# Kernel optimization log

Hardware: AMD Instinct MI355X
Metric: run time of the kernel (lower is better)

## Reference

```python
import jax, jax.numpy as jnp
import numpy as np

LEAKY_SLOPE = 0.2
ALPHA, BETA = 1.0, 0.1
CLAMP_MAX = 40.0

N_NODES, N_FEAT = 20000, 128
N_EDGES, N_QUERY = 320000, 200000
B = 512            # boundary matrix size
DIM = 8            # 'dimension' hyperparam


def setup_inputs() -> dict:
    key = jax.random.key(0)
    ks = jax.random.split(key, 20)
    sc = 1.0 / np.sqrt(B)
    inp = {
        'x': jax.random.normal(ks[0], (N_NODES, N_FEAT), jnp.float32),
        'L0': jax.random.normal(ks[1], (B, B), jnp.float32) * sc,
        'L1': jax.random.normal(ks[2], (B, B), jnp.float32) * sc,
        'edge_index': jax.random.randint(ks[3], (2, N_EDGES), 0, N_NODES),
        'total_edges': jax.random.randint(ks[4], (N_QUERY, 2), 0, N_NODES),
        # learned params (Linear weights stored as [in, out])
        'conv1_W': jax.random.normal(ks[5], (N_FEAT, 64), jnp.float32) * 0.05,
        'conv1_b': jnp.zeros((64,), jnp.float32),
        'conv2_W': jax.random.normal(ks[6], (64, 32), jnp.float32) * 0.05,
        'conv2_b': jnp.zeros((32,), jnp.float32),
        'weights_sim': jax.random.normal(ks[7], (2 * B, DIM), jnp.float32) * 0.05,
        'embeddings_sim': jax.random.normal(ks[8], (N_FEAT, 2 * B), jnp.float32) * 0.05,
        'weights_off_diagonal': jax.random.normal(ks[9], (B, B), jnp.float32) * sc,
        'weights_L_0': jax.random.normal(ks[10], (B, 32), jnp.float32) * 0.05,
        'weights_L_1': jax.random.normal(ks[11], (B, 32), jnp.float32) * 0.05,
        'lin1_W': jax.random.normal(ks[12], (DIM + 32, 32), jnp.float32) * 0.1,
        'lin1_b': jnp.zeros((32,), jnp.float32),
        'lin_W': jax.random.normal(ks[13], (32, 1), jnp.float32) * 0.1,
        'lin_b': jnp.zeros((1,), jnp.float32),
    }
    return inp


def _renorm_rows(v):
    # torch renorm_(2, 0, 1): rescale rows whose L2 norm exceeds 1
    n = jnp.linalg.norm(v, axis=1, keepdims=True)
    return v * jnp.where(n > 1.0, 1.0 / (n + 1e-7), 1.0)


def _gcn_conv(h, src, dst, dinv, W, b):
    h = h @ W
    msg = h[src] * (dinv[src] * dinv[dst])[:, None]
    return jax.ops.segment_sum(msg, dst, num_segments=h.shape[0]) + b


def reference(x, L0, L1, edge_index, total_edges,
              conv1_W, conv1_b, conv2_W, conv2_b,
              weights_sim, embeddings_sim, weights_off_diagonal,
              weights_L_0, weights_L_1, lin1_W, lin1_b, lin_W, lin_b):
    N = x.shape[0]
    # --- g_encode: two GCN layers (eval mode, dropout = identity) ---
    loops = jnp.arange(N)
    src = jnp.concatenate([edge_index[0], loops])
    dst = jnp.concatenate([edge_index[1], loops])
    deg = jax.ops.segment_sum(jnp.ones_like(dst, dtype=x.dtype), dst, num_segments=N)
    dinv = jnp.where(deg > 0, jax.lax.rsqrt(jnp.maximum(deg, 1.0)), 0.0)
    h = jax.nn.relu(_gcn_conv(x, src, dst, dinv, conv1_W, conv1_b))
    g_emb = jax.nn.relu(_gcn_conv(h, src, dst, dinv, conv2_W, conv2_b))  # [N, 32]

    # --- s_encode: boundary-matrix block + softmax ---
    L0_r = L0 @ L0
    L1_r = L1 @ L1
    rel = (L0_r @ weights_L_0) @ (L1_r @ weights_L_1).T          # [B, B]
    rel_ = weights_off_diagonal @ rel                             # [B, B]
    upper = jnp.concatenate([L0_r, rel_], axis=1)
    lower = jnp.concatenate([rel_.T, L1_r], axis=1)
    sim_block = jax.nn.softmax(jax.nn.relu(jnp.concatenate([upper, lower], axis=0)), axis=1)  # [2B, 2B]

    s_emb = ((x @ embeddings_sim) @ sim_block) @ weights_sim      # [N, DIM]
    s_emb = _renorm_rows(s_emb)
    g = _renorm_rows(g_emb)

    # --- edge gather + distance MLP ---
    i0, i1 = total_edges[:, 0], total_edges[:, 1]
    d_sim = jnp.square(s_emb[i0] - s_emb[i1])                     # [Eq, DIM]
    g_sq = jnp.square(g[i0] - g[i1])                              # [Eq, 32]
    feat = jnp.concatenate([ALPHA * g_sq, BETA * d_sim], axis=1)  # [Eq, 40]
    hq = jax.nn.leaky_relu(feat @ lin1_W + lin1_b, LEAKY_SLOPE)
    sqdist = jnp.abs(hq @ lin_W + lin_b).reshape(-1)
    sqdist = jnp.clip(sqdist, 0.0, CLAMP_MAX)
    prob = jax.nn.sigmoid(2.0 - sqdist)  # == 1/(exp(sqdist-2)+1)
    return prob
```

## Files before the change

kernel.cpp:

```cpp
#include <hip/hip_runtime.h>
#include <math.h>

#define NE 320000
#define NN 20000
#define NQ 200000

struct Prm {
  const float *x, *L0, *L1;
  const int *ei, *te;
  const float *W1, *b1, *W2, *b2, *wsim, *embs, *wod, *wL0, *wL1, *lin1W, *lin1b, *linW, *linb;
  float *out;
  int *ideg, *start, *cursor, *csr;
  float *dinv, *h1raw, *h2raw, *g, *L0r, *L1r, *T0, *T1, *S0, *Bb, *Ab2, *Mm, *Ee, *semb, *Cpart;
};

__device__ __forceinline__ void gemm512_part(char* smem, const float* __restrict__ A,
                                             const float* __restrict__ B,
                                             float* __restrict__ C, int bb, int kbase) {
  float (*As)[68] = (float(*)[68])smem;
  float (*Bs)[68] = (float(*)[68])(smem + 16 * 68 * 4);
  int tid = threadIdx.x;
  int tx = tid & 15, ty = tid >> 4;
  int brow = (bb >> 3) * 64;
  int bcol = (bb & 7) * 64;
  float c[4][4] = {};
  for (int k0 = kbase; k0 < kbase + 128; k0 += 16) {
#pragma unroll
    for (int t = 0; t < 4; t++) {
      int idx = tid * 4 + t;
      int r = idx >> 4, cc = idx & 15;
      As[cc][r] = A[(size_t)(brow + r) * 512 + k0 + cc];
      int r2 = idx >> 6, c2 = idx & 63;
      Bs[r2][c2] = B[(size_t)(k0 + r2) * 512 + bcol + c2];
    }
    __syncthreads();
#pragma unroll
    for (int k = 0; k < 16; k++) {
      float a0 = As[k][ty * 4 + 0], a1 = As[k][ty * 4 + 1];
      float a2 = As[k][ty * 4 + 2], a3 = As[k][ty * 4 + 3];
      float b0 = Bs[k][tx * 4 + 0], b1 = Bs[k][tx * 4 + 1];
      float b2 = Bs[k][tx * 4 + 2], b3 = Bs[k][tx * 4 + 3];
      c[0][0] = fmaf(a0, b0, c[0][0]); c[0][1] = fmaf(a0, b1, c[0][1]);
      c[0][2] = fmaf(a0, b2, c[0][2]); c[0][3] = fmaf(a0, b3, c[0][3]);
      c[1][0] = fmaf(a1, b0, c[1][0]); c[1][1] = fmaf(a1, b1, c[1][1]);
      c[1][2] = fmaf(a1, b2, c[1][2]); c[1][3] = fmaf(a1, b3, c[1][3]);
      c[2][0] = fmaf(a2, b0, c[2][0]); c[2][1] = fmaf(a2, b1, c[2][1]);
      c[2][2] = fmaf(a2, b2, c[2][2]); c[2][3] = fmaf(a2, b3, c[2][3]);
      c[3][0] = fmaf(a3, b0, c[3][0]); c[3][1] = fmaf(a3, b1, c[3][1]);
      c[3][2] = fmaf(a3, b2, c[3][2]); c[3][3] = fmaf(a3, b3, c[3][3]);
    }
    __syncthreads();
  }
#pragma unroll
  for (int i = 0; i < 4; i++)
#pragma unroll
    for (int j = 0; j < 4; j++)
      C[(size_t)(brow + ty * 4 + i) * 512 + bcol + tx * 4 + j] = c[i][j];
}

template<int K, int N>
__device__ __forceinline__ void xw_stream(const float* __restrict__ X,
                                          const float* __restrict__ W,
                                          float* __restrict__ Y, int bb, int M) {
  constexpr int TPR = N / 4;
  constexpr int ROWS = 256 / TPR;
  int r = bb * ROWS + threadIdx.x / TPR;
  int c4 = (threadIdx.x % TPR) * 4;
  if (r >= M) return;
  const float4* xr4 = (const float4*)(X + (size_t)r * K);
  float a0 = 0, a1 = 0, a2 = 0, a3 = 0;
#pragma unroll 4
  for (int k4 = 0; k4 < K / 4; k4++) {
    float4 xv = xr4[k4];
    int kb = k4 * 4;
    { const float4 w = *(const float4*)&W[(kb + 0) * N + c4];
      a0 = fmaf(xv.x, w.x, a0); a1 = fmaf(xv.x, w.y, a1); a2 = fmaf(xv.x, w.z, a2); a3 = fmaf(xv.x, w.w, a3); }
    { const float4 w = *(const float4*)&W[(kb + 1) * N + c4];
      a0 = fmaf(xv.y, w.x, a0); a1 = fmaf(xv.y, w.y, a1); a2 = fmaf(xv.y, w.z, a2); a3 = fmaf(xv.y, w.w, a3); }
    { const float4 w = *(const float4*)&W[(kb + 2) * N + c4];
      a0 = fmaf(xv.z, w.x, a0); a1 = fmaf(xv.z, w.y, a1); a2 = fmaf(xv.z, w.z, a2); a3 = fmaf(xv.z, w.w, a3); }
    { const float4 w = *(const float4*)&W[(kb + 3) * N + c4];
      a0 = fmaf(xv.w, w.x, a0); a1 = fmaf(xv.w, w.y, a1); a2 = fmaf(xv.w, w.z, a2); a3 = fmaf(xv.w, w.w, a3); }
  }
  float4 o; o.x = a0; o.y = a1; o.z = a2; o.w = a3;
  *(float4*)&Y[(size_t)r * N + c4] = o;
}

__device__ __forceinline__ void sk512_body(const float* X, const float* W, float* Y, int b) {
  int r = b * 32 + threadIdx.x / 8;
  int c4 = (threadIdx.x % 8) * 4;
  const float4* xr4 = (const float4*)(X + (size_t)r * 512);
  float a0 = 0, a1 = 0, a2 = 0, a3 = 0;
#pragma unroll 2
  for (int k4 = 0; k4 < 128; k4++) {
    float4 xv = xr4[k4];
    int kb = k4 * 4;
    { const float4 w = *(const float4*)&W[(kb + 0) * 32 + c4];
      a0 = fmaf(xv.x, w.x, a0); a1 = fmaf(xv.x, w.y, a1); a2 = fmaf(xv.x, w.z, a2); a3 = fmaf(xv.x, w.w, a3); }
    { const float4 w = *(const float4*)&W[(kb + 1) * 32 + c4];
      a0 = fmaf(xv.y, w.x, a0); a1 = fmaf(xv.y, w.y, a1); a2 = fmaf(xv.y, w.z, a2); a3 = fmaf(xv.y, w.w, a3); }
    { const float4 w = *(const float4*)&W[(kb + 2) * 32 + c4];
      a0 = fmaf(xv.z, w.x, a0); a1 = fmaf(xv.z, w.y, a1); a2 = fmaf(xv.z, w.z, a2); a3 = fmaf(xv.z, w.w, a3); }
    { const float4 w = *(const float4*)&W[(kb + 3) * 32 + c4];
      a0 = fmaf(xv.w, w.x, a0); a1 = fmaf(xv.w, w.y, a1); a2 = fmaf(xv.w, w.z, a2); a3 = fmaf(xv.w, w.w, a3); }
  }
  float4 o; o.x = a0; o.y = a1; o.z = a2; o.w = a3;
  *(float4*)&Y[(size_t)r * 32 + c4] = o;
}


__global__ __launch_bounds__(256) void k1(Prm p) {
  __shared__ __align__(16) char smem[8704];
  int b = blockIdx.x;
  if (b < 512) {
    int slice = b & 3, tile = (b >> 2) & 63, g = b >> 8;
    const float* A = g ? p.L1 : p.L0;
    float* C = p.Cpart + (size_t)slice * 524288 + (size_t)g * 262144;
    gemm512_part(smem, A, A, C, tile, slice * 128);
  }
  else if (b < 528)  sk512_body(p.L0, p.wL0, p.T0, b - 512);
  else if (b < 544)  sk512_body(p.L1, p.wL1, p.T1, b - 528);
  else if (b < 1794) xw_stream<128, 64>(p.x, p.W1, p.h1raw, b - 544, NN);
  else {
    int e = (b - 1794) * 256 + threadIdx.x;
    if (e < NE) atomicAdd(&p.ideg[p.ei[NE + e]], 1);
  }
}

__global__ __launch_bounds__(256) void k2(Prm p) {
  int b = blockIdx.x;
  int tid = threadIdx.x;
  if (b < 512) {
    int i4 = b * 256 + tid;
    const float4* cp = (const float4*)p.Cpart;
    float4 a = cp[i4];
    float4 b1 = cp[131072 + i4];
    float4 c = cp[262144 + i4];
    float4 d = cp[393216 + i4];
    float4 o;
    o.x = a.x + b1.x + c.x + d.x;
    o.y = a.y + b1.y + c.y + d.y;
    o.z = a.z + b1.z + c.z + d.z;
    o.w = a.w + b1.w + c.w + d.w;
    ((float4*)p.L0r)[i4] = o;
    return;
  }
  if (b < 528) { sk512_body(p.L0, p.T0, p.S0, b - 512); return; }
  if (b < 544) { sk512_body(p.L1, p.T1, p.Bb, b - 528); return; }
  __shared__ int wsum[4];
  int base = tid * 80;
  int4 c[20];
  int s = 0;
  if (base < NN) {
    const int4* ip = (const int4*)p.ideg + tid * 20;
#pragma unroll
    for (int i = 0; i < 20; i++) c[i] = ip[i];
#pragma unroll
    for (int i = 0; i < 20; i++) s += c[i].x + c[i].y + c[i].z + c[i].w;
  }
  int lane = tid & 63, wid = tid >> 6;
  int v = s;
#pragma unroll
  for (int o = 1; o < 64; o <<= 1) { int u = __shfl_up(v, o); if (lane >= o) v += u; }
  if (lane == 63) wsum[wid] = v;
  __syncthreads();
  int wbase = 0;
  for (int w = 0; w < wid; w++) wbase += wsum[w];
  int off = wbase + v - s;
  if (base < NN) {
#pragma unroll
    for (int i = 0; i < 20; i++) {
      int4 cc = c[i];
      int4 st;
      st.x = off; off += cc.x;
      st.y = off; off += cc.y;
      st.z = off; off += cc.z;
      st.w = off; off += cc.w;
      ((int4*)p.start)[tid * 20 + i] = st;
      ((int4*)p.cursor)[tid * 20 + i] = st;
      float4 dv;
      dv.x = rsqrtf((float)(cc.x + 1));
      dv.y = rsqrtf((float)(cc.y + 1));
      dv.z = rsqrtf((float)(cc.z + 1));
      dv.w = rsqrtf((float)(cc.w + 1));
      ((float4*)p.dinv)[tid * 20 + i] = dv;
    }
  }
}

__global__ __launch_bounds__(256) void k3(Prm p) {
  int b = blockIdx.x;
  if (b < 16) { sk512_body(p.wod, p.S0, p.Ab2, b); return; }
  int e = (b - 16) * 256 + threadIdx.x;
  if (e < NE) {
    int d = p.ei[NE + e];
    int pos = atomicAdd(&p.cursor[d], 1);
    p.csr[pos] = p.ei[e];
  }
}

__global__ __launch_bounds__(256) void k4(Prm p) {
  int i = blockIdx.x;
  int tid = threadIdx.x;
  __shared__ float smax[4];
  __shared__ float sred[4][9];
  float urow[32];
  {
    const float4* up = (const float4*)((i < 512) ? (p.Ab2 + i * 32) : (p.Bb + (i - 512) * 32));
#pragma unroll
    for (int q = 0; q < 8; q++) {
      float4 u4 = up[q];
      urow[q * 4 + 0] = u4.x; urow[q * 4 + 1] = u4.y;
      urow[q * 4 + 2] = u4.z; urow[q * 4 + 3] = u4.w;
    }
  }
  float loc[4];
  float mymax = 0.0f;
#pragma unroll
  for (int tt = 0; tt < 4; tt++) {
    int j = tid + tt * 256;
    float v;
    if (i < 512) {
      if (j < 512) v = p.L0r[i * 512 + j];
      else {
        const float4* bj = (const float4*)(p.Bb + (j - 512) * 32);
        float acc = 0.0f;
#pragma unroll
        for (int q = 0; q < 8; q++) {
          float4 b4 = bj[q];
          acc = fmaf(urow[q * 4 + 0], b4.x, acc); acc = fmaf(urow[q * 4 + 1], b4.y, acc);
          acc = fmaf(urow[q * 4 + 2], b4.z, acc); acc = fmaf(urow[q * 4 + 3], b4.w, acc);
        }
        v = acc;
      }
    } else {
      int r = i - 512;
      if (j < 512) {
        const float4* aj = (const float4*)(p.Ab2 + j * 32);
        float acc = 0.0f;
#pragma unroll
        for (int q = 0; q < 8; q++) {
          float4 a4 = aj[q];
          acc = fmaf(urow[q * 4 + 0], a4.x, acc); acc = fmaf(urow[q * 4 + 1], a4.y, acc);
          acc = fmaf(urow[q * 4 + 2], a4.z, acc); acc = fmaf(urow[q * 4 + 3], a4.w, acc);
        }
        v = acc;
      } else v = p.L1r[r * 512 + (j - 512)];
    }
    v = fmaxf(v, 0.0f);
    loc[tt] = v;
    mymax = fmaxf(mymax, v);
  }
#pragma unroll
  for (int o = 32; o > 0; o >>= 1) mymax = fmaxf(mymax, __shfl_down(mymax, o));
  int wid = tid >> 6, lane = tid & 63;
  if (lane == 0) smax[wid] = mymax;
  __syncthreads();
  float m = fmaxf(fmaxf(smax[0], smax[1]), fmaxf(smax[2], smax[3]));

  float z = 0.0f, pm[8] = {};
#pragma unroll
  for (int tt = 0; tt < 4; tt++) {
    int j = tid + tt * 256;
    float e = __expf(loc[tt] - m);
    z += e;
    const float* wr = p.wsim + j * 8;
#pragma unroll
    for (int d = 0; d < 8; d++) pm[d] = fmaf(e, wr[d], pm[d]);
  }
#pragma unroll
  for (int o = 32; o > 0; o >>= 1) {
    z += __shfl_down(z, o);
#pragma unroll
    for (int d = 0; d < 8; d++) pm[d] += __shfl_down(pm[d], o);
  }
  if (lane == 0) {
    sred[wid][0] = z;
#pragma unroll
    for (int d = 0; d < 8; d++) sred[wid][1 + d] = pm[d];
  }
  __syncthreads();
  if (tid < 8) {
    float zt = sred[0][0] + sred[1][0] + sred[2][0] + sred[3][0];
    float pt = sred[0][1 + tid] + sred[1][1 + tid] + sred[2][1 + tid] + sred[3][1 + tid];
    p.Mm[i * 8 + tid] = pt / zt;
  }
}

__global__ __launch_bounds__(256) void k5(Prm p) {
  __shared__ float W2l[64 * 32];
  __shared__ float h1l[4][64];
  int b = blockIdx.x;
  int tid = threadIdx.x;
  if (b < 5000) {
    for (int u = tid; u < 512; u += 256)
      ((float4*)W2l)[u] = ((const float4*)p.W2)[u];
    __syncthreads();
    int w = tid >> 6;
    int lane = tid & 63;
    int slot = lane >> 4;
    int fi = lane & 15;
    int n = b * 4 + w;
    int s0 = p.start[n], cnt = p.ideg[n];
    float4 acc = {0.f, 0.f, 0.f, 0.f};
    for (int k = 0; k < cnt; k += 4) {
      int kk = k + slot;
      bool valid = kk < cnt;
      int src = valid ? p.csr[s0 + kk] : n;
      float wgt = valid ? p.dinv[src] : 0.0f;
      float4 v = ((const float4*)(p.h1raw + (size_t)src * 64))[fi];
      acc.x = fmaf(v.x, wgt, acc.x); acc.y = fmaf(v.y, wgt, acc.y);
      acc.z = fmaf(v.z, wgt, acc.z); acc.w = fmaf(v.w, wgt, acc.w);
    }
    acc.x += __shfl_xor(acc.x, 16); acc.y += __shfl_xor(acc.y, 16);
    acc.z += __shfl_xor(acc.z, 16); acc.w += __shfl_xor(acc.w, 16);
    acc.x += __shfl_xor(acc.x, 32); acc.y += __shfl_xor(acc.y, 32);
    acc.z += __shfl_xor(acc.z, 32); acc.w += __shfl_xor(acc.w, 32);
    float dn = p.dinv[n];
    float4 self = ((const float4*)(p.h1raw + (size_t)n * 64))[fi];
    float4 b1q = ((const float4*)p.b1)[fi];
    float4 h;
    h.x = fmaxf(fmaf(acc.x, dn, self.x * dn * dn) + b1q.x, 0.0f);
    h.y = fmaxf(fmaf(acc.y, dn, self.y * dn * dn) + b1q.y, 0.0f);
    h.z = fmaxf(fmaf(acc.z, dn, self.z * dn * dn) + b1q.z, 0.0f);
    h.w = fmaxf(fmaf(acc.w, dn, self.w * dn * dn) + b1q.w, 0.0f);
    if (slot == 0) ((float4*)h1l[w])[fi] = h;
    __syncthreads();
    int c = lane & 31, half = lane >> 5;
    float s = 0.0f;
    const float* hr = h1l[w];
#pragma unroll
    for (int kk2 = 0; kk2 < 32; kk2++) {
      int k = half * 32 + kk2;
      s = fmaf(hr[k], W2l[k * 32 + c], s);
    }
    s += __shfl_xor(s, 32);
    if (half == 0) p.h2raw[(size_t)n * 32 + c] = s;
    return;
  }
  int lane = tid & 63;
  int r = (b - 5000) * 4 + (tid >> 6);
  const float* er = p.embs + (size_t)r * 1024;
  float acc[8] = {};
  for (int it = 0; it < 16; it++) {
    int k = lane + it * 64;
    float e = er[k];
    const float4* mp = (const float4*)&p.Mm[k * 8];
    float4 m0 = mp[0], m1 = mp[1];
    acc[0] = fmaf(e, m0.x, acc[0]); acc[1] = fmaf(e, m0.y, acc[1]);
    acc[2] = fmaf(e, m0.z, acc[2]); acc[3] = fmaf(e, m0.w, acc[3]);
    acc[4] = fmaf(e, m1.x, acc[4]); acc[5] = fmaf(e, m1.y, acc[5]);
    acc[6] = fmaf(e, m1.z, acc[6]); acc[7] = fmaf(e, m1.w, acc[7]);
  }
#pragma unroll
  for (int o = 32; o > 0; o >>= 1)
#pragma unroll
    for (int d = 0; d < 8; d++) acc[d] += __shfl_down(acc[d], o);
  if (lane == 0)
#pragma unroll
    for (int d = 0; d < 8; d++) p.Ee[r * 8 + d] = acc[d];
}

__global__ __launch_bounds__(256) void k6(Prm p) {
  __shared__ float El[1024];
  int b = blockIdx.x;
  int tid = threadIdx.x;
  if (b < 5000) {
    int w = tid >> 6;
    int lane = tid & 63;
    int slot = lane >> 3;
    int fi = lane & 7;
    int n = b * 4 + w;
    int s0 = p.start[n], cnt = p.ideg[n];
    float4 acc = {0.f, 0.f, 0.f, 0.f};
    for (int k = 0; k < cnt; k += 8) {
      int kk = k + slot;
      bool valid = kk < cnt;
      int src = valid ? p.csr[s0 + kk] : n;
      float wgt = valid ? p.dinv[src] : 0.0f;
      float4 v = ((const float4*)(p.h2raw + (size_t)src * 32))[fi];
      acc.x = fmaf(v.x, wgt, acc.x); acc.y = fmaf(v.y, wgt, acc.y);
      acc.z = fmaf(v.z, wgt, acc.z); acc.w = fmaf(v.w, wgt, acc.w);
    }
    acc.x += __shfl_xor(acc.x, 8);  acc.y += __shfl_xor(acc.y, 8);
    acc.z += __shfl_xor(acc.z, 8);  acc.w += __shfl_xor(acc.w, 8);
    acc.x += __shfl_xor(acc.x, 16); acc.y += __shfl_xor(acc.y, 16);
    acc.z += __shfl_xor(acc.z, 16); acc.w += __shfl_xor(acc.w, 16);
    acc.x += __shfl_xor(acc.x, 32); acc.y += __shfl_xor(acc.y, 32);
    acc.z += __shfl_xor(acc.z, 32); acc.w += __shfl_xor(acc.w, 32);
    float dn = p.dinv[n];
    float4 self = ((const float4*)(p.h2raw + (size_t)n * 32))[fi];
    float4 b2q = ((const float4*)p.b2)[fi];
    float4 h;
    h.x = fmaxf(fmaf(acc.x, dn, self.x * dn * dn) + b2q.x, 0.0f);
    h.y = fmaxf(fmaf(acc.y, dn, self.y * dn * dn) + b2q.y, 0.0f);
    h.z = fmaxf(fmaf(acc.z, dn, self.z * dn * dn) + b2q.z, 0.0f);
    h.w = fmaxf(fmaf(acc.w, dn, self.w * dn * dn) + b2q.w, 0.0f);
    float n2 = h.x * h.x + h.y * h.y + h.z * h.z + h.w * h.w;
    n2 += __shfl_xor(n2, 1); n2 += __shfl_xor(n2, 2); n2 += __shfl_xor(n2, 4);
    float nrm = sqrtf(n2);
    float sc = (nrm > 1.0f) ? 1.0f / (nrm + 1e-7f) : 1.0f;
    if (slot == 0) {
      float4 o; o.x = h.x * sc; o.y = h.y * sc; o.z = h.z * sc; o.w = h.w * sc;
      ((float4*)(p.g + (size_t)n * 32))[fi] = o;
    }
    return;
  }
  for (int u = tid; u < 256; u += 256)
    ((float4*)El)[u] = ((const float4*)p.Ee)[u];
  __syncthreads();
  int row = (b - 5000) * 256 + tid;
  if (row >= NN) return;
  const float4* xr4 = (const float4*)(p.x + (size_t)row * 128);
  float s[8] = {};
#pragma unroll 4
  for (int k4 = 0; k4 < 32; k4++) {
    float4 xv = xr4[k4];
    int kb = k4 * 4;
#pragma unroll
    for (int u = 0; u < 4; u++) {
      float xk = (u == 0) ? xv.x : (u == 1) ? xv.y : (u == 2) ? xv.z : xv.w;
      const float4* ep = (const float4*)&El[(kb + u) * 8];
      float4 e0 = ep[0], e1 = ep[1];
      s[0] = fmaf(xk, e0.x, s[0]); s[1] = fmaf(xk, e0.y, s[1]);
      s[2] = fmaf(xk, e0.z, s[2]); s[3] = fmaf(xk, e0.w, s[3]);
      s[4] = fmaf(xk, e1.x, s[4]); s[5] = fmaf(xk, e1.y, s[5]);
      s[6] = fmaf(xk, e1.z, s[6]); s[7] = fmaf(xk, e1.w, s[7]);
    }
  }
  float n2 = 0.0f;
#pragma unroll
  for (int d = 0; d < 8; d++) n2 += s[d] * s[d];
  float n = sqrtf(n2);
  float sc = (n > 1.0f) ? 1.0f / (n + 1e-7f) : 1.0f;
#pragma unroll
  for (int d = 0; d < 8; d++) p.semb[(size_t)row * 8 + d] = s[d] * sc;
}

__global__ __launch_bounds__(256) void k7(Prm p) {
  int q = blockIdx.x * 256 + threadIdx.x;
  if (q >= NQ) return;
  const int2 pr = ((const int2*)p.te)[q];
  int i0 = pr.x, i1 = pr.y;
  float feat[40];
  const float4* g0 = (const float4*)(p.g + (size_t)i0 * 32);
  const float4* g1 = (const float4*)(p.g + (size_t)i1 * 32);
#pragma unroll
  for (int u = 0; u < 8; u++) {
    float4 a = g0[u], b = g1[u];
    float d0 = a.x - b.x, d1 = a.y - b.y, d2 = a.z - b.z, d3 = a.w - b.w;
    feat[u * 4 + 0] = d0 * d0; feat[u * 4 + 1] = d1 * d1;
    feat[u * 4 + 2] = d2 * d2; feat[u * 4 + 3] = d3 * d3;
  }
  const float4* s0 = (const float4*)(p.semb + (size_t)i0 * 8);
  const float4* s1 = (const float4*)(p.semb + (size_t)i1 * 8);
#pragma unroll
  for (int u = 0; u < 2; u++) {
    float4 a = s0[u], b = s1[u];
    float d0 = a.x - b.x, d1 = a.y - b.y, d2 = a.z - b.z, d3 = a.w - b.w;
    feat[32 + u * 4 + 0] = 0.1f * d0 * d0; feat[32 + u * 4 + 1] = 0.1f * d1 * d1;
    feat[32 + u * 4 + 2] = 0.1f * d2 * d2; feat[32 + u * 4 + 3] = 0.1f * d3 * d3;
  }
  float acc[32];
#pragma unroll
  for (int c = 0; c < 32; c++) acc[c] = p.lin1b[c];
#pragma unroll
  for (int k = 0; k < 40; k++) {
    float f = feat[k];
#pragma unroll
    for (int c = 0; c < 32; c++) acc[c] = fmaf(f, p.lin1W[k * 32 + c], acc[c]);
  }
  float accv = p.linb[0];
#pragma unroll
  for (int c = 0; c < 32; c++) {
    float a = acc[c];
    a = (a > 0.0f) ? a : 0.2f * a;
    accv = fmaf(a, p.linW[c], accv);
  }
  float sq = fminf(fabsf(accv), 40.0f);
  p.out[q] = 1.0f / (1.0f + __expf(sq - 2.0f));
}

extern "C" void kernel_launch(void* const* d_in, const int* in_sizes, int n_in,
                              void* d_out, int out_size, void* d_ws, size_t ws_size,
                              hipStream_t stream) {
  Prm p;
  p.x     = (const float*)d_in[0];
  p.L0    = (const float*)d_in[1];
  p.L1    = (const float*)d_in[2];
  p.ei    = (const int*)d_in[3];
  p.te    = (const int*)d_in[4];
  p.W1    = (const float*)d_in[5];
  p.b1    = (const float*)d_in[6];
  p.W2    = (const float*)d_in[7];
  p.b2    = (const float*)d_in[8];
  p.wsim  = (const float*)d_in[9];
  p.embs  = (const float*)d_in[10];
  p.wod   = (const float*)d_in[11];
  p.wL0   = (const float*)d_in[12];
  p.wL1   = (const float*)d_in[13];
  p.lin1W = (const float*)d_in[14];
  p.lin1b = (const float*)d_in[15];
  p.linW  = (const float*)d_in[16];
  p.linb  = (const float*)d_in[17];
  p.out   = (float*)d_out;

  p.ideg   = (int*)d_ws;
  p.start  = p.ideg + 20000;
  p.cursor = p.start + 20000;
  p.csr    = p.cursor + 20000;
  p.dinv   = (float*)(p.csr + 320000);
  p.h1raw  = p.dinv + 20000;
  p.h2raw  = p.h1raw + 1280000;
  p.g      = p.h2raw + 640000;
  p.L0r    = p.g + 640000;
  p.L1r    = p.L0r + 262144;
  p.T0     = p.L1r + 262144;
  p.T1     = p.T0 + 16384;
  p.S0     = p.T1 + 16384;
  p.Bb     = p.S0 + 16384;
  p.Ab2    = p.Bb + 16384;
  p.Mm     = p.Ab2 + 16384;
  p.Ee     = p.Mm + 8192;
  p.semb   = p.Ee + 1024;
  p.Cpart  = p.semb + 160000;

  hipMemsetAsync(p.ideg, 0, 20000 * sizeof(int), stream);
  k1<<<3044, 256, 0, stream>>>(p);
  k2<<<545,  256, 0, stream>>>(p);
  k3<<<1266, 256, 0, stream>>>(p);
  k4<<<1024, 256, 0, stream>>>(p);
  k5<<<5032, 256, 0, stream>>>(p);
  k6<<<5079, 256, 0, stream>>>(p);
  k7<<<782,  256, 0, stream>>>(p);
}
```

Measured before the change: 184.5 us.

## Reassociate wod@L0@L0 chain, fuse CSR fill into softmax kernel, stage W1 in LDS

The product wod@(L0r@T0) is reassociated as (wod@L0)@L0@T0. The wod@L0 GEMM now runs in k1 alongside the L0/L1 squaring, and its four split-K partials are summed on the fly in k2, so one dependent kernel stage disappears. The CSR scatter is merged into the softmax kernel, cutting one launch. The x@W1 stream also stages W1 chunks in shared memory. This adds 256 GEMM blocks to k1, enlarges the Cpart scratch, and slightly changes floating-point rounding order.

```diff
diff --git a/kernel.cpp b/kernel.cpp
--- a/kernel.cpp
+++ b/kernel.cpp
@@ -11,7 +11,7 @@
   const float *W1, *b1, *W2, *b2, *wsim, *embs, *wod, *wL0, *wL1, *lin1W, *lin1b, *linW, *linb;
   float *out;
   int *ideg, *start, *cursor, *csr;
-  float *dinv, *h1raw, *h2raw, *g, *L0r, *L1r, *T0, *T1, *S0, *Bb, *Ab2, *Mm, *Ee, *semb, *Cpart;
+  float *dinv, *h1raw, *h2raw, *g, *L0r, *L1r, *T0, *T1, *Bb, *Ab2, *Mm, *Ee, *semb, *Cpart;
 };
 
 __device__ __forceinline__ void gemm512_part(char* smem, const float* __restrict__ A,
@@ -58,32 +58,43 @@
       C[(size_t)(brow + ty * 4 + i) * 512 + bcol + tx * 4 + j] = c[i][j];
 }
 
-template<int K, int N>
-__device__ __forceinline__ void xw_stream(const float* __restrict__ X,
-                                          const float* __restrict__ W,
-                                          float* __restrict__ Y, int bb, int M) {
+template<int K, int N, int KC>
+__device__ __forceinline__ void xw_chunk(char* smem, const float* __restrict__ X,
+                                         const float* __restrict__ W,
+                                         float* __restrict__ Y, int bb, int M) {
   constexpr int TPR = N / 4;
   constexpr int ROWS = 256 / TPR;
+  float* Wl = (float*)smem;
   int r = bb * ROWS + threadIdx.x / TPR;
   int c4 = (threadIdx.x % TPR) * 4;
-  if (r >= M) return;
-  const float4* xr4 = (const float4*)(X + (size_t)r * K);
   float a0 = 0, a1 = 0, a2 = 0, a3 = 0;
-#pragma unroll 4
-  for (int k4 = 0; k4 < K / 4; k4++) {
-    float4 xv = xr4[k4];
-    int kb = k4 * 4;
-    { const float4 w = *(const float4*)&W[(kb + 0) * N + c4];
-      a0 = fmaf(xv.x, w.x, a0); a1 = fmaf(xv.x, w.y, a1); a2 = fmaf(xv.x, w.z, a2); a3 = fmaf(xv.x, w.w, a3); }
-    { const float4 w = *(const float4*)&W[(kb + 1) * N + c4];
-      a0 = fmaf(xv.y, w.x, a0); a1 = fmaf(xv.y, w.y, a1); a2 = fmaf(xv.y, w.z, a2); a3 = fmaf(xv.y, w.w, a3); }
-    { const float4 w = *(const float4*)&W[(kb + 2) * N + c4];
-      a0 = fmaf(xv.z, w.x, a0); a1 = fmaf(xv.z, w.y, a1); a2 = fmaf(xv.z, w.z, a2); a3 = fmaf(xv.z, w.w, a3); }
-    { const float4 w = *(const float4*)&W[(kb + 3) * N + c4];
-      a0 = fmaf(xv.w, w.x, a0); a1 = fmaf(xv.w, w.y, a1); a2 = fmaf(xv.w, w.z, a2); a3 = fmaf(xv.w, w.w, a3); }
-  }
-  float4 o; o.x = a0; o.y = a1; o.z = a2; o.w = a3;
-  *(float4*)&Y[(size_t)r * N + c4] = o;
+#pragma unroll 1
+  for (int k0 = 0; k0 < K; k0 += KC) {
+    __syncthreads();
+    for (int t = threadIdx.x; t < KC * N / 4; t += 256)
+      ((float4*)Wl)[t] = ((const float4*)(W + k0 * N))[t];
+    __syncthreads();
+    if (r < M) {
+      const float4* xr4 = (const float4*)(X + (size_t)r * K + k0);
+#pragma unroll
+      for (int k4 = 0; k4 < KC / 4; k4++) {
+        float4 xv = xr4[k4];
+        int kb = k4 * 4;
+        { const float4 w = *(const float4*)&Wl[(kb + 0) * N + c4];
+          a0 = fmaf(xv.x, w.x, a0); a1 = fmaf(xv.x, w.y, a1); a2 = fmaf(xv.x, w.z, a2); a3 = fmaf(xv.x, w.w, a3); }
+        { const float4 w = *(const float4*)&Wl[(kb + 1) * N + c4];
+          a0 = fmaf(xv.y, w.x, a0); a1 = fmaf(xv.y, w.y, a1); a2 = fmaf(xv.y, w.z, a2); a3 = fmaf(xv.y, w.w, a3); }
+        { const float4 w = *(const float4*)&Wl[(kb + 2) * N + c4];
+          a0 = fmaf(xv.z, w.x, a0); a1 = fmaf(xv.z, w.y, a1); a2 = fmaf(xv.z, w.z, a2); a3 = fmaf(xv.z, w.w, a3); }
+        { const float4 w = *(const float4*)&Wl[(kb + 3) * N + c4];
+          a0 = fmaf(xv.w, w.x, a0); a1 = fmaf(xv.w, w.y, a1); a2 = fmaf(xv.w, w.z, a2); a3 = fmaf(xv.w, w.w, a3); }
+      }
+    }
+  }
+  if (r < M) {
+    float4 o; o.x = a0; o.y = a1; o.z = a2; o.w = a3;
+    *(float4*)&Y[(size_t)r * N + c4] = o;
+  }
 }
 
 __device__ __forceinline__ void sk512_body(const float* X, const float* W, float* Y, int b) {
@@ -108,21 +119,55 @@
   *(float4*)&Y[(size_t)r * 32 + c4] = o;
 }
 
+__device__ __forceinline__ void sk512_sum4(const float* Xbase, size_t sstride4,
+                                           const float* W, float* Y, int b) {
+  int r = b * 32 + threadIdx.x / 8;
+  int c4 = (threadIdx.x % 8) * 4;
+  const float4* x0 = (const float4*)Xbase + (size_t)r * 128;
+  float a0 = 0, a1 = 0, a2 = 0, a3 = 0;
+#pragma unroll 2
+  for (int k4 = 0; k4 < 128; k4++) {
+    float4 xa = x0[k4];
+    float4 xb = x0[sstride4 + k4];
+    float4 xc = x0[2 * sstride4 + k4];
+    float4 xd = x0[3 * sstride4 + k4];
+    float4 xv;
+    xv.x = xa.x + xb.x + xc.x + xd.x;
+    xv.y = xa.y + xb.y + xc.y + xd.y;
+    xv.z = xa.z + xb.z + xc.z + xd.z;
+    xv.w = xa.w + xb.w + xc.w + xd.w;
+    int kb = k4 * 4;
+    { const float4 w = *(const float4*)&W[(kb + 0) * 32 + c4];
+      a0 = fmaf(xv.x, w.x, a0); a1 = fmaf(xv.x, w.y, a1); a2 = fmaf(xv.x, w.z, a2); a3 = fmaf(xv.x, w.w, a3); }
+    { const float4 w = *(const float4*)&W[(kb + 1) * 32 + c4];
+      a0 = fmaf(xv.y, w.x, a0); a1 = fmaf(xv.y, w.y, a1); a2 = fmaf(xv.y, w.z, a2); a3 = fmaf(xv.y, w.w, a3); }
+    { const float4 w = *(const float4*)&W[(kb + 2) * 32 + c4];
+      a0 = fmaf(xv.z, w.x, a0); a1 = fmaf(xv.z, w.y, a1); a2 = fmaf(xv.z, w.z, a2); a3 = fmaf(xv.z, w.w, a3); }
+    { const float4 w = *(const float4*)&W[(kb + 3) * 32 + c4];
+      a0 = fmaf(xv.w, w.x, a0); a1 = fmaf(xv.w, w.y, a1); a2 = fmaf(xv.w, w.z, a2); a3 = fmaf(xv.w, w.w, a3); }
+  }
+  float4 o; o.x = a0; o.y = a1; o.z = a2; o.w = a3;
+  *(float4*)&Y[(size_t)r * 32 + c4] = o;
+}
+
+#define CP_G 262144
+#define CP_S 786432
 
 __global__ __launch_bounds__(256) void k1(Prm p) {
   __shared__ __align__(16) char smem[8704];
   int b = blockIdx.x;
-  if (b < 512) {
+  if (b < 768) {
     int slice = b & 3, tile = (b >> 2) & 63, g = b >> 8;
-    const float* A = g ? p.L1 : p.L0;
-    float* C = p.Cpart + (size_t)slice * 524288 + (size_t)g * 262144;
-    gemm512_part(smem, A, A, C, tile, slice * 128);
-  }
-  else if (b < 528)  sk512_body(p.L0, p.wL0, p.T0, b - 512);
-  else if (b < 544)  sk512_body(p.L1, p.wL1, p.T1, b - 528);
-  else if (b < 1794) xw_stream<128, 64>(p.x, p.W1, p.h1raw, b - 544, NN);
+    const float* A = (g == 0) ? p.L0 : (g == 1) ? p.L1 : p.wod;
+    const float* B = (g == 1) ? p.L1 : p.L0;
+    float* C = p.Cpart + (size_t)slice * CP_S + (size_t)g * CP_G;
+    gemm512_part(smem, A, B, C, tile, slice * 128);
+  }
+  else if (b < 784)  sk512_body(p.L0, p.wL0, p.T0, b - 768);
+  else if (b < 800)  sk512_body(p.L1, p.wL1, p.T1, b - 784);
+  else if (b < 2050) xw_chunk<128, 64, 32>(smem, p.x, p.W1, p.h1raw, b - 800, NN);
   else {
-    int e = (b - 1794) * 256 + threadIdx.x;
+    int e = (b - 2050) * 256 + threadIdx.x;
     if (e < NE) atomicAdd(&p.ideg[p.ei[NE + e]], 1);
   }
 }
@@ -134,9 +179,9 @@
     int i4 = b * 256 + tid;
     const float4* cp = (const float4*)p.Cpart;
     float4 a = cp[i4];
-    float4 b1 = cp[131072 + i4];
-    float4 c = cp[262144 + i4];
-    float4 d = cp[393216 + i4];
+    float4 b1 = cp[CP_S / 4 + i4];
+    float4 c = cp[2 * (CP_S / 4) + i4];
+    float4 d = cp[3 * (CP_S / 4) + i4];
     float4 o;
     o.x = a.x + b1.x + c.x + d.x;
     o.y = a.y + b1.y + c.y + d.y;
@@ -145,7 +190,7 @@
     ((float4*)p.L0r)[i4] = o;
     return;
   }
-  if (b < 528) { sk512_body(p.L0, p.T0, p.S0, b - 512); return; }
+  if (b < 528) { sk512_sum4(p.Cpart + 2 * CP_G, CP_S / 4, p.T0, p.Ab2, b - 512); return; }
   if (b < 544) { sk512_body(p.L1, p.T1, p.Bb, b - 528); return; }
   __shared__ int wsum[4];
   int base = tid * 80;
@@ -190,18 +235,17 @@
 
 __global__ __launch_bounds__(256) void k3(Prm p) {
   int b = blockIdx.x;
-  if (b < 16) { sk512_body(p.wod, p.S0, p.Ab2, b); return; }
-  int e = (b - 16) * 256 + threadIdx.x;
-  if (e < NE) {
-    int d = p.ei[NE + e];
-    int pos = atomicAdd(&p.cursor[d], 1);
-    p.csr[pos] = p.ei[e];
-  }
-}
-
-__global__ __launch_bounds__(256) void k4(Prm p) {
-  int i = blockIdx.x;
   int tid = threadIdx.x;
+  if (b >= 1024) {
+    int e = (b - 1024) * 256 + tid;
+    if (e < NE) {
+      int d = p.ei[NE + e];
+      int pos = atomicAdd(&p.cursor[d], 1);
+      p.csr[pos] = p.ei[e];
+    }
+    return;
+  }
+  int i = b;
   __shared__ float smax[4];
   __shared__ float sred[4][9];
   float urow[32];
@@ -287,7 +331,7 @@
   }
 }
 
-__global__ __launch_bounds__(256) void k5(Prm p) {
+__global__ __launch_bounds__(256) void k4(Prm p) {
   __shared__ float W2l[64 * 32];
   __shared__ float h1l[4][64];
   int b = blockIdx.x;
@@ -361,7 +405,7 @@
     for (int d = 0; d < 8; d++) p.Ee[r * 8 + d] = acc[d];
 }
 
-__global__ __launch_bounds__(256) void k6(Prm p) {
+__global__ __launch_bounds__(256) void k5(Prm p) {
   __shared__ float El[1024];
   int b = blockIdx.x;
   int tid = threadIdx.x;
@@ -437,7 +481,7 @@
   for (int d = 0; d < 8; d++) p.semb[(size_t)row * 8 + d] = s[d] * sc;
 }
 
-__global__ __launch_bounds__(256) void k7(Prm p) {
+__global__ __launch_bounds__(256) void k6(Prm p) {
   int q = blockIdx.x * 256 + threadIdx.x;
   if (q >= NQ) return;
   const int2 pr = ((const int2*)p.te)[q];
@@ -517,8 +561,7 @@
   p.L1r    = p.L0r + 262144;
   p.T0     = p.L1r + 262144;
   p.T1     = p.T0 + 16384;
-  p.S0     = p.T1 + 16384;
-  p.Bb     = p.S0 + 16384;
+  p.Bb     = p.T1 + 16384;
   p.Ab2    = p.Bb + 16384;
   p.Mm     = p.Ab2 + 16384;
   p.Ee     = p.Mm + 8192;
@@ -526,11 +569,10 @@
   p.Cpart  = p.semb + 160000;
 
   hipMemsetAsync(p.ideg, 0, 20000 * sizeof(int), stream);
-  k1<<<3044, 256, 0, stream>>>(p);
+  k1<<<3300, 256, 0, stream>>>(p);
   k2<<<545,  256, 0, stream>>>(p);
-  k3<<<1266, 256, 0, stream>>>(p);
-  k4<<<1024, 256, 0, stream>>>(p);
-  k5<<<5032, 256, 0, stream>>>(p);
-  k6<<<5079, 256, 0, stream>>>(p);
-  k7<<<782,  256, 0, stream>>>(p);
-}
+  k3<<<2274, 256, 0, stream>>>(p);
+  k4<<<5032, 256, 0, stream>>>(p);
+  k5<<<5079, 256, 0, stream>>>(p);
+  k6<<<782,  256, 0, stream>>>(p);
+}
```

After: 165.5 us. -10.3%, faster.
